# Kernel tuning notes

Hardware: AMD Instinct MI355X
Metric: run time of the kernel (lower is better)

The kernel has to match this reference:

```python
import jax, jax.numpy as jnp
from jax import lax
import numpy as np

NUM_CENTROIDS = 1024
RADIUS = 0.5
K = 32
EPS = 1e-5


def _fps(xyz, num_samples):
    """Farthest point sampling. Deterministic start at index 0 (torch uses randint)."""
    B, N, _ = xyz.shape

    def step(carry, _):
        distances, farthest = carry
        centroid = jnp.take_along_axis(xyz, farthest[:, None, None], axis=1)  # [B,1,3]
        d = jnp.sum((xyz - centroid) ** 2, axis=-1)  # [B,N]
        distances = jnp.minimum(distances, d)
        nxt = jnp.argmax(distances, axis=-1).astype(jnp.int32)
        return (distances, nxt), farthest

    init = (jnp.full((B, N), jnp.inf, dtype=xyz.dtype), jnp.zeros((B,), jnp.int32))
    _, idxs = lax.scan(step, init, None, length=num_samples)  # [M,B]
    return jnp.transpose(idxs)  # [B,M]


def _ball_query(xyz, new_xyz):
    """K nearest neighbors within RADIUS; out-of-ball slots fall back to nearest."""
    d2 = (jnp.sum(new_xyz ** 2, -1)[:, :, None] + jnp.sum(xyz ** 2, -1)[:, None, :]
          - 2.0 * jnp.einsum('bmd,bnd->bmn', new_xyz, xyz))
    dist = jnp.sqrt(jnp.maximum(d2, 0.0))  # [B,M,N] cdist
    dist = jnp.where(dist > RADIUS, jnp.inf, dist)
    neg_vals, idx = lax.top_k(-dist, K)  # smallest-K distances
    mask = jnp.isinf(neg_vals)  # outside radius
    idx = jnp.where(mask, idx[:, :, 0:1], idx)
    return idx  # [B,M,K]


def _forward(xyz, features, Ws, bs, gs, bts):
    B, N, _ = xyz.shape
    cidx = lax.stop_gradient(_fps(xyz, NUM_CENTROIDS))  # [B,M] int
    new_xyz = jnp.take_along_axis(xyz, cidx[:, :, None], axis=1)  # [B,M,3]
    gidx = lax.stop_gradient(_ball_query(xyz, new_xyz))  # [B,M,K] int
    flat = gidx.reshape(B, -1)
    gxyz = jnp.take_along_axis(xyz, flat[:, :, None], axis=1).reshape(B, NUM_CENTROIDS, K, 3)
    gxyz = gxyz - new_xyz[:, :, None, :]
    gfeat = jnp.take_along_axis(features, flat[:, :, None], axis=1).reshape(B, NUM_CENTROIDS, K, -1)
    h = jnp.concatenate([gxyz, gfeat], axis=-1)  # [B,M,K,C+3]
    for W, b, g, bt in zip(Ws, bs, gs, bts):
        # 1x1 Conv1d == per-point linear over channels
        h = jnp.einsum('bmkc,oc->bmko', h, W) + b
        # BatchNorm1d in training mode: batch stats over (B*M, K), biased var
        mu = jnp.mean(h, axis=(0, 1, 2))
        var = jnp.var(h, axis=(0, 1, 2))
        h = (h - mu) * lax.rsqrt(var + EPS) * g + bt
        h = jax.nn.gelu(h, approximate=False)  # torch nn.GELU default (exact erf)
    return new_xyz, jnp.max(h, axis=2)  # [B,M,3], [B,M,128]


def setup_inputs() -> dict:
    key = jax.random.key(0)
    ks = jax.random.split(key, 8)
    B, N, C = 8, 8192, 64
    xyz = jax.random.normal(ks[0], (B, N, 3), jnp.float32)
    features = jax.random.normal(ks[1], (B, N, C), jnp.float32)
    chans = [C + 3, 64, 64, 128]
    inp = {"xyz": xyz, "features": features}
    for l in range(3):
        cin, cout = chans[l], chans[l + 1]
        inp[f"W{l + 1}"] = jax.random.normal(ks[2 + l], (cout, cin), jnp.float32) / jnp.float32(np.sqrt(cin))
        inp[f"b{l + 1}"] = jnp.zeros((cout,), jnp.float32)
        inp[f"g{l + 1}"] = jnp.ones((cout,), jnp.float32)
        inp[f"bt{l + 1}"] = jnp.zeros((cout,), jnp.float32)
    return inp


def reference(xyz, features, W1, b1, g1, bt1, W2, b2, g2, bt2, W3, b3, g3, bt3):
    return _forward(xyz, features, (W1, W2, W3), (b1, b2, b3), (g1, g2, g3), (bt1, bt2, bt3))
```

## Files before the change

kernel.cpp:

```cpp
#include <hip/hip_runtime.h>
#include <cstdint>
#include <cstddef>

#define BATCH 8
#define NPTS  8192
#define MCENT 1024
#define KNN   32
#define CFEAT 64
#define EPS_F 1e-5f

#define WS_NEED 73400320ull

__device__ __forceinline__ float erf_fast(float x) {
  float a = fabsf(x);
  float t = __builtin_amdgcn_rcpf(fmaf(0.3275911f, a, 1.0f));
  float p = fmaf(1.061405429f, t, -1.453152027f);
  p = fmaf(p, t, 1.421413741f);
  p = fmaf(p, t, -0.284496736f);
  p = fmaf(p, t, 0.254829592f);
  float e = __expf(-a * a);
  float y = fmaf(-p * t, e, 1.0f);
  return copysignf(y, x);
}
__device__ __forceinline__ float gelu_f(float x) {
  return 0.5f * x * (1.0f + erf_fast(x * 0.70710678118654752440f));
}

template<int CTRL>
__device__ __forceinline__ float dpp_max_step(float v) {
  int s = __builtin_amdgcn_update_dpp(__float_as_int(v), __float_as_int(v),
                                      CTRL, 0xf, 0xf, false);
  return fmaxf(v, __int_as_float(s));
}
__device__ __forceinline__ float wave_max_dpp(float v) {
  v = dpp_max_step<0x111>(v);
  v = dpp_max_step<0x112>(v);
  v = dpp_max_step<0x114>(v);
  v = dpp_max_step<0x118>(v);
  v = dpp_max_step<0x142>(v);
  v = dpp_max_step<0x143>(v);
  return v;
}
template<int CTRL>
__device__ __forceinline__ unsigned long long dpp_min64_step(unsigned long long v) {
  int lo = __builtin_amdgcn_update_dpp((int)(unsigned)(v & 0xffffffffull),
                                       (int)(unsigned)(v & 0xffffffffull),
                                       CTRL, 0xf, 0xf, false);
  int hi = __builtin_amdgcn_update_dpp((int)(unsigned)(v >> 32),
                                       (int)(unsigned)(v >> 32),
                                       CTRL, 0xf, 0xf, false);
  unsigned long long o = (((unsigned long long)(unsigned)hi) << 32) | (unsigned)lo;
  return o < v ? o : v;
}
__device__ __forceinline__ unsigned long long wave_min64_dpp(unsigned long long v) {
  v = dpp_min64_step<0x111>(v);
  v = dpp_min64_step<0x112>(v);
  v = dpp_min64_step<0x114>(v);
  v = dpp_min64_step<0x118>(v);
  v = dpp_min64_step<0x142>(v);
  v = dpp_min64_step<0x143>(v);
  return v;
}

#define FPS_STEPS 64
__global__ __launch_bounds__(512, 1) void fps_phase_kernel(
    const float* __restrict__ xyz, float* __restrict__ new_xyz,
    float* __restrict__ dist_ws, float* __restrict__ cst, int s0)
{
  __shared__ float pts[NPTS * 3];
  __shared__ float outb[FPS_STEPS * 3];
  __shared__ unsigned long long keys[2][8];
  int b = blockIdx.x, t = threadIdx.x;
  const float* xb = xyz + (size_t)b * NPTS * 3;

  float px[16], py[16], pz[16], dist[16];
  {
    const float4* src = (const float4*)(xb + (size_t)t * 48);
    float4 buf[12];
#pragma unroll
    for (int i = 0; i < 12; ++i) buf[i] = src[i];
    const float* f = (const float*)buf;
#pragma unroll
    for (int i = 0; i < 16; ++i) {
      px[i] = f[i*3+0]; py[i] = f[i*3+1]; pz[i] = f[i*3+2];
    }
    float4* dst = (float4*)(pts + (size_t)t * 48);
#pragma unroll
    for (int i = 0; i < 12; ++i) dst[i] = buf[i];
  }
  float* dw = dist_ws + (size_t)b * NPTS + (size_t)t * 16;
  float cx, cy, cz;
  if (s0 == 0) {
#pragma unroll
    for (int i = 0; i < 16; ++i) dist[i] = __builtin_inff();
    cx = xb[0]; cy = xb[1]; cz = xb[2];
  } else {
    float4 d0 = *(const float4*)(dw + 0);
    float4 d1 = *(const float4*)(dw + 4);
    float4 d2 = *(const float4*)(dw + 8);
    float4 d3 = *(const float4*)(dw + 12);
    dist[0]=d0.x; dist[1]=d0.y; dist[2]=d0.z; dist[3]=d0.w;
    dist[4]=d1.x; dist[5]=d1.y; dist[6]=d1.z; dist[7]=d1.w;
    dist[8]=d2.x; dist[9]=d2.y; dist[10]=d2.z; dist[11]=d2.w;
    dist[12]=d3.x; dist[13]=d3.y; dist[14]=d3.z; dist[15]=d3.w;
    cx = cst[b*3+0]; cy = cst[b*3+1]; cz = cst[b*3+2];
  }
  int lane = t & 63, wv = t >> 6;

  for (int s = 0; s < FPS_STEPS; ++s) {
    if (t == 0) { outb[s*3+0] = cx; outb[s*3+1] = cy; outb[s*3+2] = cz; }
    float bd = -1.0f; int bslot = 0;
#pragma unroll
    for (int i = 0; i < 16; ++i) {
      float dx = __fsub_rn(px[i], cx);
      float dy = __fsub_rn(py[i], cy);
      float dz = __fsub_rn(pz[i], cz);
      float d  = __fadd_rn(__fadd_rn(__fmul_rn(dx,dx), __fmul_rn(dy,dy)), __fmul_rn(dz,dz));
      float nd = fminf(dist[i], d);
      dist[i] = nd;
      if (nd > bd) { bd = nd; bslot = i; }
    }
    float w = wave_max_dpp(bd);
    float wmax = __int_as_float(__builtin_amdgcn_readlane(__float_as_int(w), 63));
    unsigned long long mk = __ballot(bd == wmax);
    int sl = __ffsll((long long)mk) - 1;
    int widx = __builtin_amdgcn_readlane(t * 16 + bslot, sl);
    if (lane == 0)
      keys[s & 1][wv] = (((unsigned long long)__float_as_uint(wmax)) << 32)
                        | (unsigned)(8191 - widx);
    __syncthreads();
    unsigned long long bk = keys[s & 1][0];
#pragma unroll
    for (int w2 = 1; w2 < 8; ++w2) {
      unsigned long long o = keys[s & 1][w2];
      if (o > bk) bk = o;
    }
    int idx = 8191 - (int)(unsigned)(bk & 0xffffffffull);
    cx = pts[idx*3+0]; cy = pts[idx*3+1]; cz = pts[idx*3+2];
  }

  *(float4*)(dw + 0)  = make_float4(dist[0], dist[1], dist[2], dist[3]);
  *(float4*)(dw + 4)  = make_float4(dist[4], dist[5], dist[6], dist[7]);
  *(float4*)(dw + 8)  = make_float4(dist[8], dist[9], dist[10], dist[11]);
  *(float4*)(dw + 12) = make_float4(dist[12], dist[13], dist[14], dist[15]);
  if (t == 0) { cst[b*3+0] = cx; cst[b*3+1] = cy; cst[b*3+2] = cz; }
  __syncthreads();
  float* ob = new_xyz + (size_t)b * MCENT * 3 + (size_t)s0 * 3;
  for (int i = t; i < FPS_STEPS * 3; i += 512) ob[i] = outb[i];
}

#define BQCAP 512
__global__ __launch_bounds__(256) void bq_kernel(const float* __restrict__ xyz,
                                                 const float* __restrict__ new_xyz,
                                                 int* __restrict__ gidx)
{
  __shared__ unsigned long long list[4][BQCAP];
  int wv = threadIdx.x >> 6, lane = threadIdx.x & 63;
  int gm = blockIdx.x * 4 + wv;
  int b  = gm >> 10;
  const float* c = new_xyz + (size_t)gm * 3;
  float c0 = c[0], c1 = c[1], c2 = c[2];
  float sc = __fadd_rn(__fadd_rn(__fmul_rn(c0,c0), __fmul_rn(c1,c1)), __fmul_rn(c2,c2));
  const float* xb = xyz + (size_t)b * NPTS * 3;

  unsigned cnt = 0;
  for (int j0 = 0; j0 < NPTS; j0 += 64) {
    int j = j0 + lane;
    float x = xb[j*3+0], y = xb[j*3+1], z = xb[j*3+2];
    float sx  = __fadd_rn(__fadd_rn(__fmul_rn(x,x), __fmul_rn(y,y)), __fmul_rn(z,z));
    float dot = __fadd_rn(__fadd_rn(__fmul_rn(c0,x), __fmul_rn(c1,y)), __fmul_rn(c2,z));
    float d2  = __fsub_rn(__fadd_rn(sc, sx), __fmul_rn(2.0f, dot));
    float dist = sqrtf(fmaxf(d2, 0.0f));
    bool in_ = (dist <= 0.5f);
    unsigned long long mask = __ballot(in_);
    unsigned off = (unsigned)__popcll(mask & ((1ull << lane) - 1ull));
    if (in_) {
      unsigned pos = cnt + off;
      if (pos < BQCAP)
        list[wv][pos] = (((unsigned long long)__float_as_uint(dist)) << 32) | (unsigned)j;
    }
    cnt += (unsigned)__popcll(mask);
  }
  if (cnt > BQCAP) cnt = BQCAP;

  unsigned long long e[8];
#pragma unroll
  for (int i = 0; i < 8; ++i) {
    unsigned pos = (unsigned)lane + ((unsigned)i << 6);
    e[i] = (pos < cnt) ? list[wv][pos] : ~0ull;
  }
#define CE_(a_, b_) { bool sw = e[b_] < e[a_]; \
                      unsigned long long lo_ = sw ? e[b_] : e[a_]; \
                      unsigned long long hi_ = sw ? e[a_] : e[b_]; \
                      e[a_] = lo_; e[b_] = hi_; }
  CE_(0,1) CE_(2,3) CE_(4,5) CE_(6,7)
  CE_(0,2) CE_(1,3) CE_(4,6) CE_(5,7)
  CE_(1,2) CE_(5,6)
  CE_(0,4) CE_(1,5) CE_(2,6) CE_(3,7)
  CE_(2,4) CE_(3,5)
  CE_(1,2) CE_(3,4) CE_(5,6)
#undef CE_

  int* gout = gidx + (size_t)gm * KNN;
  int first = 0;
  int kmax = (cnt < (unsigned)KNN) ? (int)cnt : KNN;
  for (int k = 0; k < KNN; ++k) {
    if (k < kmax) {
      unsigned long long wr = wave_min64_dpp(e[0]);
      unsigned lo32 = (unsigned)__builtin_amdgcn_readlane((int)(unsigned)(wr & 0xffffffffull), 63);
      unsigned hi32 = (unsigned)__builtin_amdgcn_readlane((int)(unsigned)(wr >> 32), 63);
      unsigned long long wmin = (((unsigned long long)hi32) << 32) | lo32;
      int idxv = (int)lo32;
      if (k == 0) first = idxv;
      if (lane == 0) gout[k] = idxv;
      bool win = (e[0] == wmin);
#pragma unroll
      for (int i = 0; i < 7; ++i) e[i] = win ? e[i+1] : e[i];
      e[7] = win ? ~0ull : e[7];
    } else {
      if (lane == 0) gout[k] = first;
    }
  }
}

__global__ __launch_bounds__(256) void l1_kernel(
    const float* __restrict__ xyz, const float* __restrict__ feats,
    const float* __restrict__ new_xyz, const int* __restrict__ gidx,
    const float* __restrict__ W, const float* __restrict__ bv,
    float* __restrict__ hout)
{
  int p  = blockIdx.x * 256 + threadIdx.x;
  int b  = p >> 15;
  int r  = p & 32767;
  int mi = r >> 5;
  int idx = gidx[p];
  const float* cc = new_xyz + (size_t)(b*MCENT + mi) * 3;
  const float* q  = xyz + (size_t)(b*NPTS + idx) * 3;
  float in[67];
  in[0] = q[0] - cc[0];
  in[1] = q[1] - cc[1];
  in[2] = q[2] - cc[2];
  const float* fr = feats + (size_t)(b*NPTS + idx) * CFEAT;
#pragma unroll
  for (int j = 0; j < 64; j += 4) {
    float4 v = *(const float4*)(fr + j);
    in[3+j] = v.x; in[4+j] = v.y; in[5+j] = v.z; in[6+j] = v.w;
  }

  float* orow = hout + (size_t)p * 64;
  for (int o4 = 0; o4 < 16; ++o4) {
    const float* w0 = W + (size_t)(o4 * 4) * 67;
    float a0 = bv[o4*4+0], a1 = bv[o4*4+1], a2 = bv[o4*4+2], a3 = bv[o4*4+3];
#pragma unroll
    for (int j = 0; j < 67; ++j) {
      float x = in[j];
      a0 = fmaf(x, w0[j],       a0);
      a1 = fmaf(x, w0[67+j],    a1);
      a2 = fmaf(x, w0[134+j],   a2);
      a3 = fmaf(x, w0[201+j],   a3);
    }
    *(float4*)(orow + o4*4) = make_float4(a0, a1, a2, a3);
  }
}

__global__ __launch_bounds__(256) void l2_kernel(
    float* __restrict__ h, const float* __restrict__ W,
    const float* __restrict__ bv, const float* __restrict__ bnp,
    const float* __restrict__ btp)
{
  int p = blockIdx.x * 256 + threadIdx.x;
  float* row = h + (size_t)p * 64;
  float in[64];
#pragma unroll
  for (int j = 0; j < 64; j += 4) {
    float4 v = *(const float4*)(row + j);
    in[j+0] = gelu_f((v.x - bnp[j+0]) * bnp[64+j+0] + btp[j+0]);
    in[j+1] = gelu_f((v.y - bnp[j+1]) * bnp[64+j+1] + btp[j+1]);
    in[j+2] = gelu_f((v.z - bnp[j+2]) * bnp[64+j+2] + btp[j+2]);
    in[j+3] = gelu_f((v.w - bnp[j+3]) * bnp[64+j+3] + btp[j+3]);
  }
  for (int o4 = 0; o4 < 16; ++o4) {
    const float* w0 = W + (size_t)(o4 * 4) * 64;
    float a0 = bv[o4*4+0], a1 = bv[o4*4+1], a2 = bv[o4*4+2], a3 = bv[o4*4+3];
#pragma unroll
    for (int j = 0; j < 64; ++j) {
      float x = in[j];
      a0 = fmaf(x, w0[j],      a0);
      a1 = fmaf(x, w0[64+j],   a1);
      a2 = fmaf(x, w0[128+j],  a2);
      a3 = fmaf(x, w0[192+j],  a3);
    }
    *(float4*)(row + o4*4) = make_float4(a0, a1, a2, a3);
  }
}

template<int C>
__global__ __launch_bounds__(256) void stats_kernel(const float* __restrict__ h,
                                                    float* __restrict__ part)
{
  constexpr int G = 256 / C;
  int t = threadIdx.x;
  int c = t % C, g = t / C;
  const float* base = h + (size_t)blockIdx.x * 512 * C;
  float s = 0.0f, ss = 0.0f;
  for (int r = g; r < 512; r += G) {
    float v = base[(size_t)r * C + c];
    s += v;
    ss = fmaf(v, v, ss);
  }
  __shared__ float ls[256], lss[256];
  ls[t] = s; lss[t] = ss;
  __syncthreads();
  if (g == 0) {
    for (int gg = 1; gg < G; ++gg) { s += ls[gg*C + c]; ss += lss[gg*C + c]; }
    part[(size_t)blockIdx.x * (2*C) + c]     = s;
    part[(size_t)blockIdx.x * (2*C) + C + c] = ss;
  }
}

template<int C>
__global__ __launch_bounds__(256) void fin_kernel(const float* __restrict__ part,
                                                  const float* __restrict__ gv,
                                                  float* __restrict__ bn)
{
  int c = blockIdx.x, t = threadIdx.x;
  float s = 0.0f, ss = 0.0f;
  for (int b2 = t; b2 < 512; b2 += 256) {
    s  += part[(size_t)b2 * (2*C) + c];
    ss += part[(size_t)b2 * (2*C) + C + c];
  }
  __shared__ float ls[256], lss[256];
  ls[t] = s; lss[t] = ss;
  __syncthreads();
  for (int k = 128; k > 0; k >>= 1) {
    if (t < k) { ls[t] += ls[t+k]; lss[t] += lss[t+k]; }
    __syncthreads();
  }
  if (t == 0) {
    const float inv_n = 1.0f / 262144.0f;
    float mu  = ls[0] * inv_n;
    float var = fmaxf(lss[0] * inv_n - mu * mu, 0.0f);
    bn[c]     = mu;
    bn[C + c] = gv[c] / sqrtf(var + EPS_F);
  }
}

__global__ __launch_bounds__(256) void l3stats_kernel(
    const float* __restrict__ h2, const float* __restrict__ W3,
    const float* __restrict__ b3, const float* __restrict__ bnp,
    const float* __restrict__ btp, float* __restrict__ part)
{
  int t = threadIdx.x;
  int gb = blockIdx.x >> 1, og0 = (blockIdx.x & 1) * 64;
  int p = gb * 256 + t;
  const float* row = h2 + (size_t)p * 64;
  float in[64];
#pragma unroll
  for (int j = 0; j < 64; j += 4) {
    float4 v = *(const float4*)(row + j);
    in[j+0] = gelu_f((v.x - bnp[j+0]) * bnp[64+j+0] + btp[j+0]);
    in[j+1] = gelu_f((v.y - bnp[j+1]) * bnp[64+j+1] + btp[j+1]);
    in[j+2] = gelu_f((v.z - bnp[j+2]) * bnp[64+j+2] + btp[j+2]);
    in[j+3] = gelu_f((v.w - bnp[j+3]) * bnp[64+j+3] + btp[j+3]);
  }
  float s_[64], q_[64];
  for (int o4 = 0; o4 < 16; ++o4) {
    const float* w0 = W3 + (size_t)(og0 + o4 * 4) * 64;
    float a0 = b3[og0+o4*4+0], a1 = b3[og0+o4*4+1], a2 = b3[og0+o4*4+2], a3 = b3[og0+o4*4+3];
#pragma unroll
    for (int j = 0; j < 64; ++j) {
      float x = in[j];
      a0 = fmaf(x, w0[j],      a0);
      a1 = fmaf(x, w0[64+j],   a1);
      a2 = fmaf(x, w0[128+j],  a2);
      a3 = fmaf(x, w0[192+j],  a3);
    }
    int o = o4 * 4;
    s_[o]=a0; s_[o+1]=a1; s_[o+2]=a2; s_[o+3]=a3;
    q_[o]=a0*a0; q_[o+1]=a1*a1; q_[o+2]=a2*a2; q_[o+3]=a3*a3;
  }

  int wv = t >> 6, lane = t & 63;
#pragma unroll
  for (int st = 0; st < 6; ++st) {
    int m = 1 << st;
    bool up = (lane & m) != 0;
    int half = 32 >> st;
#pragma unroll
    for (int j = 0; j < 32; ++j) {
      if (j >= half) break;
      float ks = up ? s_[j+half] : s_[j];
      float ds = up ? s_[j]      : s_[j+half];
      s_[j] = ks + __shfl_xor(ds, m, 64);
      float kq = up ? q_[j+half] : q_[j];
      float dq = up ? q_[j]      : q_[j+half];
      q_[j] = kq + __shfl_xor(dq, m, 64);
    }
  }
  int ch = __brev((unsigned)lane) >> 26;
  float* pw = part + ((size_t)blockIdx.x * 4 + wv) * 128;
  pw[ch]      = s_[0];
  pw[64 + ch] = q_[0];
}

__global__ __launch_bounds__(256) void fin3_kernel(const float* __restrict__ part,
                                                   const float* __restrict__ gv,
                                                   float* __restrict__ bn)
{
  int c = blockIdx.x, t = threadIdx.x;
  int half = c >> 6, j = c & 63;
  float s = 0.0f, ss = 0.0f;
  for (int gb = t; gb < 1024; gb += 256) {
    int blk = gb * 2 + half;
#pragma unroll
    for (int wv = 0; wv < 4; ++wv) {
      const float* pw = part + ((size_t)blk * 4 + wv) * 128;
      s  += pw[j];
      ss += pw[64 + j];
    }
  }
  __shared__ float ls[256], lss[256];
  ls[t] = s; lss[t] = ss;
  __syncthreads();
  for (int k = 128; k > 0; k >>= 1) {
    if (t < k) { ls[t] += ls[t+k]; lss[t] += lss[t+k]; }
    __syncthreads();
  }
  if (t == 0) {
    const float inv_n = 1.0f / 262144.0f;
    float mu  = ls[0] * inv_n;
    float var = fmaxf(lss[0] * inv_n - mu * mu, 0.0f);
    bn[c]       = mu;
    bn[128 + c] = gv[c] / sqrtf(var + EPS_F);
  }
}

__global__ __launch_bounds__(256) void pool3_kernel(
    const float* __restrict__ h2, const float* __restrict__ W3,
    const float* __restrict__ b3, const float* __restrict__ bnp2,
    const float* __restrict__ btp2,
    const float* __restrict__ bnp3,
    const float* __restrict__ btp3,
    float* __restrict__ out1)
{
  int t = threadIdx.x;
  int gb = blockIdx.x >> 1, og0 = (blockIdx.x & 1) * 64;
  int p = gb * 256 + t;
  const float* row = h2 + (size_t)p * 64;
  float in[64];
#pragma unroll
  for (int j = 0; j < 64; j += 4) {
    float4 v = *(const float4*)(row + j);
    in[j+0] = gelu_f((v.x - bnp2[j+0]) * bnp2[64+j+0] + btp2[j+0]);
    in[j+1] = gelu_f((v.y - bnp2[j+1]) * bnp2[64+j+1] + btp2[j+1]);
    in[j+2] = gelu_f((v.z - bnp2[j+2]) * bnp2[64+j+2] + btp2[j+2]);
    in[j+3] = gelu_f((v.w - bnp2[j+3]) * bnp2[64+j+3] + btp2[j+3]);
  }
  float g_[64];
  for (int o4 = 0; o4 < 16; ++o4) {
    const float* w0 = W3 + (size_t)(og0 + o4 * 4) * 64;
    float a0 = b3[og0+o4*4+0], a1 = b3[og0+o4*4+1], a2 = b3[og0+o4*4+2], a3 = b3[og0+o4*4+3];
#pragma unroll
    for (int j = 0; j < 64; ++j) {
      float x = in[j];
      a0 = fmaf(x, w0[j],      a0);
      a1 = fmaf(x, w0[64+j],   a1);
      a2 = fmaf(x, w0[128+j],  a2);
      a3 = fmaf(x, w0[192+j],  a3);
    }
    int oc0 = og0 + o4 * 4, o = o4 * 4;
    g_[o]   = gelu_f((a0 - bnp3[oc0+0]) * bnp3[128+oc0+0] + btp3[oc0+0]);
    g_[o+1] = gelu_f((a1 - bnp3[oc0+1]) * bnp3[128+oc0+1] + btp3[oc0+1]);
    g_[o+2] = gelu_f((a2 - bnp3[oc0+2]) * bnp3[128+oc0+2] + btp3[oc0+2]);
    g_[o+3] = gelu_f((a3 - bnp3[oc0+3]) * bnp3[128+oc0+3] + btp3[oc0+3]);
  }

#pragma unroll
  for (int st = 0; st < 5; ++st) {
    int m = 1 << st;
    bool up = (t & m) != 0;
    int half = 32 >> st;
#pragma unroll
    for (int j = 0; j < 32; ++j) {
      if (j >= half) break;
      float k = up ? g_[j+half] : g_[j];
      float d = up ? g_[j]      : g_[j+half];
      g_[j] = fmaxf(k, __shfl_xor(d, m, 64));
    }
  }
  int ch0 = (int)(__brev((unsigned)(t & 31)) >> 27) * 2;
  int gm = gb * 8 + (t >> 5);
  out1[(size_t)gm * 128 + og0 + ch0]     = g_[0];
  out1[(size_t)gm * 128 + og0 + ch0 + 1] = g_[1];
}

__global__ void fill_kernel(float* __restrict__ out1) {
  out1[blockIdx.x * 256 + threadIdx.x] = 1.0e6f;
}

extern "C" void kernel_launch(void* const* d_in, const int* in_sizes, int n_in,
                              void* d_out, int out_size, void* d_ws, size_t ws_size,
                              hipStream_t stream)
{
  (void)in_sizes; (void)n_in; (void)out_size;
  const float* xyz   = (const float*)d_in[0];
  const float* feats = (const float*)d_in[1];
  const float* W1  = (const float*)d_in[2];
  const float* b1  = (const float*)d_in[3];
  const float* g1  = (const float*)d_in[4];
  const float* bt1 = (const float*)d_in[5];
  const float* W2  = (const float*)d_in[6];
  const float* b2  = (const float*)d_in[7];
  const float* g2  = (const float*)d_in[8];
  const float* bt2 = (const float*)d_in[9];
  const float* W3  = (const float*)d_in[10];
  const float* b3  = (const float*)d_in[11];
  const float* g3  = (const float*)d_in[12];
  const float* bt3 = (const float*)d_in[13];

  float* out0 = (float*)d_out;
  float* out1 = out0 + (size_t)BATCH * MCENT * 3;

  char* ws = (char*)d_ws;
  int*   gidx    = (int*)(ws + 0);
  float* part    = (float*)(ws + (1u << 20));
  float* bn0     = (float*)(ws + 5u * (1u << 20));
  float* bn1     = bn0 + 128;
  float* bn2     = bn0 + 256;
  float* dist_ws = (float*)(ws + 5u * (1u << 20) + 65536u);
  float* cst     = (float*)(ws + 5u * (1u << 20) + 65536u + 262144u);
  float* h1      = (float*)(ws + 6u * (1u << 20));

  if (ws_size < WS_NEED) {
    fill_kernel<<<4096, 256, 0, stream>>>(out1);
    return;
  }

  for (int ph = 0; ph < MCENT / FPS_STEPS; ++ph)
    fps_phase_kernel<<<BATCH, 512, 0, stream>>>(xyz, out0, dist_ws, cst,
                                                ph * FPS_STEPS);

  bq_kernel<<<2048, 256, 0, stream>>>(xyz, out0, gidx);
  l1_kernel<<<1024, 256, 0, stream>>>(xyz, feats, out0, gidx, W1, b1, h1);
  stats_kernel<64><<<512, 256, 0, stream>>>(h1, part);
  fin_kernel<64><<<64, 256, 0, stream>>>(part, g1, bn0);
  l2_kernel<<<1024, 256, 0, stream>>>(h1, W2, b2, bn0, bt1);
  stats_kernel<64><<<512, 256, 0, stream>>>(h1, part);
  fin_kernel<64><<<64, 256, 0, stream>>>(part, g2, bn1);
  l3stats_kernel<<<2048, 256, 0, stream>>>(h1, W3, b3, bn1, bt2, part);
  fin3_kernel<<<128, 256, 0, stream>>>(part, g3, bn2);
  pool3_kernel<<<2048, 256, 0, stream>>>(h1, W3, b3, bn1, bt2, bn2, bt3, out1);
}
```

Measured before the change: 1.708 ms.

## Precompute layer-2 BN+GELU once and split layer-3 output channels into quarters

Adds an act_kernel that applies BN2 and GELU to h1 in place, so the layer-3 stats and pool kernels no longer each recompute erf-based GELU on the 64 inputs. Layer-3 kernels now cover 32 output channels per block across 4096 blocks instead of 64 across 2048. This cuts per-thread register arrays and the shuffle-tree depth, and the partial-sum layout and fin3 indexing are adjusted to match. The cost is an extra read and write pass over the 64 MB activation buffer plus one more launch.

```diff
diff --git a/kernel.cpp b/kernel.cpp
--- a/kernel.cpp
+++ b/kernel.cpp
@@ -60,6 +60,30 @@
   v = dpp_min64_step<0x142>(v);
   v = dpp_min64_step<0x143>(v);
   return v;
+}
+
+template<int M, int HALF>
+__device__ __forceinline__ void tree_step(float* s_, float* q_, int lane) {
+  bool up = (lane & M) != 0;
+#pragma unroll
+  for (int j = 0; j < HALF; ++j) {
+    float ks = up ? s_[j+HALF] : s_[j];
+    float ds = up ? s_[j]      : s_[j+HALF];
+    s_[j] = ks + __shfl_xor(ds, M, 64);
+    float kq = up ? q_[j+HALF] : q_[j];
+    float dq = up ? q_[j]      : q_[j+HALF];
+    q_[j] = kq + __shfl_xor(dq, M, 64);
+  }
+}
+template<int M, int HALF>
+__device__ __forceinline__ void ptree_step(float* g_, int kbit) {
+  bool up = (kbit & M) != 0;
+#pragma unroll
+  for (int j = 0; j < HALF; ++j) {
+    float kv = up ? g_[j+HALF] : g_[j];
+    float dv = up ? g_[j]      : g_[j+HALF];
+    g_[j] = fmaxf(kv, __shfl_xor(dv, M, 64));
+  }
 }
 
 #define FPS_STEPS 64
@@ -345,26 +369,40 @@
   }
 }
 
-__global__ __launch_bounds__(256) void l3stats_kernel(
-    const float* __restrict__ h2, const float* __restrict__ W3,
-    const float* __restrict__ b3, const float* __restrict__ bnp,
-    const float* __restrict__ btp, float* __restrict__ part)
-{
-  int t = threadIdx.x;
-  int gb = blockIdx.x >> 1, og0 = (blockIdx.x & 1) * 64;
-  int p = gb * 256 + t;
-  const float* row = h2 + (size_t)p * 64;
-  float in[64];
+__global__ __launch_bounds__(256) void act_kernel(float* __restrict__ h,
+                                                  const float* __restrict__ bnp,
+                                                  const float* __restrict__ btp)
+{
+  int p = blockIdx.x * 256 + threadIdx.x;
+  float* row = h + (size_t)p * 64;
 #pragma unroll
   for (int j = 0; j < 64; j += 4) {
     float4 v = *(const float4*)(row + j);
-    in[j+0] = gelu_f((v.x - bnp[j+0]) * bnp[64+j+0] + btp[j+0]);
-    in[j+1] = gelu_f((v.y - bnp[j+1]) * bnp[64+j+1] + btp[j+1]);
-    in[j+2] = gelu_f((v.z - bnp[j+2]) * bnp[64+j+2] + btp[j+2]);
-    in[j+3] = gelu_f((v.w - bnp[j+3]) * bnp[64+j+3] + btp[j+3]);
-  }
-  float s_[64], q_[64];
-  for (int o4 = 0; o4 < 16; ++o4) {
+    v.x = gelu_f((v.x - bnp[j+0]) * bnp[64+j+0] + btp[j+0]);
+    v.y = gelu_f((v.y - bnp[j+1]) * bnp[64+j+1] + btp[j+1]);
+    v.z = gelu_f((v.z - bnp[j+2]) * bnp[64+j+2] + btp[j+2]);
+    v.w = gelu_f((v.w - bnp[j+3]) * bnp[64+j+3] + btp[j+3]);
+    *(float4*)(row + j) = v;
+  }
+}
+
+__global__ __launch_bounds__(256, 1) void l3stats_kernel(
+    const float* __restrict__ g2, const float* __restrict__ W3,
+    const float* __restrict__ b3, float* __restrict__ part)
+{
+  int t = threadIdx.x;
+  int gb = blockIdx.x >> 2, chunk = blockIdx.x & 3;
+  int og0 = chunk * 32;
+  int p = gb * 256 + t;
+  const float* row = g2 + (size_t)p * 64;
+  float in[64];
+#pragma unroll
+  for (int j = 0; j < 64; j += 4) {
+    float4 v = *(const float4*)(row + j);
+    in[j+0] = v.x; in[j+1] = v.y; in[j+2] = v.z; in[j+3] = v.w;
+  }
+  float s_[32], q_[32];
+  for (int o4 = 0; o4 < 8; ++o4) {
     const float* w0 = W3 + (size_t)(og0 + o4 * 4) * 64;
     float a0 = b3[og0+o4*4+0], a1 = b3[og0+o4*4+1], a2 = b3[og0+o4*4+2], a3 = b3[og0+o4*4+3];
 #pragma unroll
@@ -381,26 +419,17 @@
   }
 
   int wv = t >> 6, lane = t & 63;
-#pragma unroll
-  for (int st = 0; st < 6; ++st) {
-    int m = 1 << st;
-    bool up = (lane & m) != 0;
-    int half = 32 >> st;
-#pragma unroll
-    for (int j = 0; j < 32; ++j) {
-      if (j >= half) break;
-      float ks = up ? s_[j+half] : s_[j];
-      float ds = up ? s_[j]      : s_[j+half];
-      s_[j] = ks + __shfl_xor(ds, m, 64);
-      float kq = up ? q_[j+half] : q_[j];
-      float dq = up ? q_[j]      : q_[j+half];
-      q_[j] = kq + __shfl_xor(dq, m, 64);
-    }
-  }
-  int ch = __brev((unsigned)lane) >> 26;
-  float* pw = part + ((size_t)blockIdx.x * 4 + wv) * 128;
-  pw[ch]      = s_[0];
-  pw[64 + ch] = q_[0];
+  tree_step<1,16>(s_, q_, lane);
+  tree_step<2, 8>(s_, q_, lane);
+  tree_step<4, 4>(s_, q_, lane);
+  tree_step<8, 2>(s_, q_, lane);
+  tree_step<16,1>(s_, q_, lane);
+  s_[0] += __shfl_xor(s_[0], 32, 64);
+  q_[0] += __shfl_xor(q_[0], 32, 64);
+
+  int ch = (int)(__brev((unsigned)(lane & 31)) >> 27);
+  float* pw = part + ((size_t)blockIdx.x * 4 + wv) * 64;
+  if (lane < 32) { pw[ch] = s_[0]; pw[32 + ch] = q_[0]; }
 }
 
 __global__ __launch_bounds__(256) void fin3_kernel(const float* __restrict__ part,
@@ -408,15 +437,15 @@
                                                    float* __restrict__ bn)
 {
   int c = blockIdx.x, t = threadIdx.x;
-  int half = c >> 6, j = c & 63;
+  int chunk = c >> 5, j = c & 31;
   float s = 0.0f, ss = 0.0f;
   for (int gb = t; gb < 1024; gb += 256) {
-    int blk = gb * 2 + half;
+    int blk = gb * 4 + chunk;
 #pragma unroll
     for (int wv = 0; wv < 4; ++wv) {
-      const float* pw = part + ((size_t)blk * 4 + wv) * 128;
+      const float* pw = part + ((size_t)blk * 4 + wv) * 64;
       s  += pw[j];
-      ss += pw[64 + j];
+      ss += pw[32 + j];
     }
   }
   __shared__ float ls[256], lss[256];
@@ -435,29 +464,26 @@
   }
 }
 
-__global__ __launch_bounds__(256) void pool3_kernel(
-    const float* __restrict__ h2, const float* __restrict__ W3,
-    const float* __restrict__ b3, const float* __restrict__ bnp2,
-    const float* __restrict__ btp2,
+__global__ __launch_bounds__(256, 1) void pool3_kernel(
+    const float* __restrict__ g2, const float* __restrict__ W3,
+    const float* __restrict__ b3,
     const float* __restrict__ bnp3,
     const float* __restrict__ btp3,
     float* __restrict__ out1)
 {
   int t = threadIdx.x;
-  int gb = blockIdx.x >> 1, og0 = (blockIdx.x & 1) * 64;
+  int gb = blockIdx.x >> 2, chunk = blockIdx.x & 3;
+  int og0 = chunk * 32;
   int p = gb * 256 + t;
-  const float* row = h2 + (size_t)p * 64;
+  const float* row = g2 + (size_t)p * 64;
   float in[64];
 #pragma unroll
   for (int j = 0; j < 64; j += 4) {
     float4 v = *(const float4*)(row + j);
-    in[j+0] = gelu_f((v.x - bnp2[j+0]) * bnp2[64+j+0] + btp2[j+0]);
-    in[j+1] = gelu_f((v.y - bnp2[j+1]) * bnp2[64+j+1] + btp2[j+1]);
-    in[j+2] = gelu_f((v.z - bnp2[j+2]) * bnp2[64+j+2] + btp2[j+2]);
-    in[j+3] = gelu_f((v.w - bnp2[j+3]) * bnp2[64+j+3] + btp2[j+3]);
-  }
-  float g_[64];
-  for (int o4 = 0; o4 < 16; ++o4) {
+    in[j+0] = v.x; in[j+1] = v.y; in[j+2] = v.z; in[j+3] = v.w;
+  }
+  float g_[32];
+  for (int o4 = 0; o4 < 8; ++o4) {
     const float* w0 = W3 + (size_t)(og0 + o4 * 4) * 64;
     float a0 = b3[og0+o4*4+0], a1 = b3[og0+o4*4+1], a2 = b3[og0+o4*4+2], a3 = b3[og0+o4*4+3];
 #pragma unroll
@@ -475,23 +501,15 @@
     g_[o+3] = gelu_f((a3 - bnp3[oc0+3]) * bnp3[128+oc0+3] + btp3[oc0+3]);
   }
 
-#pragma unroll
-  for (int st = 0; st < 5; ++st) {
-    int m = 1 << st;
-    bool up = (t & m) != 0;
-    int half = 32 >> st;
-#pragma unroll
-    for (int j = 0; j < 32; ++j) {
-      if (j >= half) break;
-      float k = up ? g_[j+half] : g_[j];
-      float d = up ? g_[j]      : g_[j+half];
-      g_[j] = fmaxf(k, __shfl_xor(d, m, 64));
-    }
-  }
-  int ch0 = (int)(__brev((unsigned)(t & 31)) >> 27) * 2;
+  ptree_step<1,16>(g_, t);
+  ptree_step<2, 8>(g_, t);
+  ptree_step<4, 4>(g_, t);
+  ptree_step<8, 2>(g_, t);
+  ptree_step<16,1>(g_, t);
+
+  int ch = (int)(__brev((unsigned)(t & 31)) >> 27);
   int gm = gb * 8 + (t >> 5);
-  out1[(size_t)gm * 128 + og0 + ch0]     = g_[0];
-  out1[(size_t)gm * 128 + og0 + ch0 + 1] = g_[1];
+  out1[(size_t)gm * 128 + og0 + ch] = g_[0];
 }
 
 __global__ void fill_kernel(float* __restrict__ out1) {
@@ -547,7 +565,8 @@
   l2_kernel<<<1024, 256, 0, stream>>>(h1, W2, b2, bn0, bt1);
   stats_kernel<64><<<512, 256, 0, stream>>>(h1, part);
   fin_kernel<64><<<64, 256, 0, stream>>>(part, g2, bn1);
-  l3stats_kernel<<<2048, 256, 0, stream>>>(h1, W3, b3, bn1, bt2, part);
+  act_kernel<<<1024, 256, 0, stream>>>(h1, bn1, bt2);
+  l3stats_kernel<<<4096, 256, 0, stream>>>(h1, W3, b3, part);
   fin3_kernel<<<128, 256, 0, stream>>>(part, g3, bn2);
-  pool3_kernel<<<2048, 256, 0, stream>>>(h1, W3, b3, bn1, bt2, bn2, bt3, out1);
-}
+  pool3_kernel<<<4096, 256, 0, stream>>>(h1, W3, b3, bn2, bt3, out1);
+}
```

Result: faster. 1.623 ms (-4.9%).
